# Performance work log

Hardware: AMD Instinct MI355X
Metric: run time of the kernel (lower is better)

The kernel has to match this reference:

```python
import jax, jax.numpy as jnp
import numpy as np

N = 100000   # nodes
E = 1600000  # edges (avg degree 16)
D = 128      # input feature dim
H = 128      # Config.hidden_dim
G = 64       # graphs in batch
OUT = 2      # output classes


def setup_inputs() -> dict:
    key = jax.random.key(0)
    ks = jax.random.split(key, 12)
    s = 0.05
    return {
        "x": jax.random.normal(ks[0], (N, D), dtype=jnp.float32),
        "edge_index": jax.random.randint(ks[1], (2, E), 0, N),
        "batch": jnp.sort(jax.random.randint(ks[2], (N,), 0, G)),
        "W1": jax.random.normal(ks[3], (H, D), dtype=jnp.float32) * s,
        "b1": jnp.zeros((H,), jnp.float32),
        "W2": jax.random.normal(ks[4], (H, H), dtype=jnp.float32) * s,
        "b2": jnp.zeros((H,), jnp.float32),
        "Wf1": jax.random.normal(ks[5], (H, H), dtype=jnp.float32) * s,
        "bf1": jnp.zeros((H,), jnp.float32),
        "Wf2": jax.random.normal(ks[6], (OUT, H), dtype=jnp.float32) * s,
        "bf2": jnp.zeros((OUT,), jnp.float32),
    }


def _gnn_layer(x, src, dst, W, b):
    # message(x_j) = Linear(x[src]); linear commutes with gather, so transform
    # node features once (N rows) instead of per-edge (E rows): same math.
    xw = x @ W.T + b                                   # [N, H]
    msg = xw[src]                                      # [E, H] gather
    summed = jax.ops.segment_sum(msg, dst, num_segments=N)            # [N, H]
    cnt = jax.ops.segment_sum(jnp.ones((src.shape[0],), x.dtype), dst,
                              num_segments=N)                          # [N]
    return summed / jnp.maximum(cnt, 1.0)[:, None]     # scatter-mean (0 for deg-0)


def reference(x, edge_index, batch, W1, b1, W2, b2, Wf1, bf1, Wf2, bf2):
    src, dst = edge_index[0], edge_index[1]
    h = jax.nn.relu(_gnn_layer(x, src, dst, W1, b1))
    h = jax.nn.relu(_gnn_layer(h, src, dst, W2, b2))
    g = jax.ops.segment_max(h, batch, num_segments=G)  # global_max_pool [G, H]
    z = jax.nn.relu(g @ Wf1.T + bf1)                   # fc (dropout = identity, eval)
    z = z @ Wf2.T + bf2                                # [G, OUT]
    return jax.nn.log_softmax(z, axis=1)
```

## Files before the change

kernel.cpp:

```cpp
#include <hip/hip_runtime.h>
#include <hip/hip_fp16.h>
#include <math.h>


#define SPLIT 16
#define BUCKET_SHIFT 8
#define BUCKET_SIZE 256
#define MAXBUCK 512
#define BIN_CHUNK 4096
#define CAP 4608
#define LSTR 136

typedef _Float16 half8 __attribute__((ext_vector_type(8)));
typedef _Float16 half4v __attribute__((ext_vector_type(4)));
typedef float floatx4 __attribute__((ext_vector_type(4)));
typedef float floatx2 __attribute__((ext_vector_type(2)));

__global__ void k_init(int* bcur, int* gstart, int* gend, int G, int nbuck) {
    int i = threadIdx.x;
    if (i < nbuck) bcur[i] = i * CAP;
    if (i < G) { gstart[i] = 0; gend[i] = 0; }
}

__global__ void k_bin(const int* __restrict__ src, const int* __restrict__ dst,
                      int* __restrict__ bcur, int* __restrict__ staging,
                      const int* __restrict__ batch, int* __restrict__ gstart,
                      int* __restrict__ gend, int E, int N, int nbuck) {
    __shared__ int lh[MAXBUCK];
    __shared__ int lbase[MAXBUCK];
    __shared__ int lc[MAXBUCK];
    int gid = blockIdx.x * blockDim.x + threadIdx.x;
    if (gid < N) {
        int b = batch[gid];
        if (gid == 0 || batch[gid - 1] != b) gstart[b] = gid;
        if (gid == N - 1 || batch[gid + 1] != b) gend[b] = gid + 1;
    }
    for (int i = threadIdx.x; i < nbuck; i += blockDim.x) { lh[i] = 0; lc[i] = 0; }
    __syncthreads();
    int base = blockIdx.x * BIN_CHUNK;
    int end = min(base + BIN_CHUNK, E);
    for (int e = base + threadIdx.x; e < end; e += blockDim.x)
        atomicAdd(&lh[dst[e] >> BUCKET_SHIFT], 1);
    __syncthreads();
    for (int i = threadIdx.x; i < nbuck; i += blockDim.x)
        if (lh[i]) lbase[i] = atomicAdd(&bcur[i], lh[i]);
    __syncthreads();
    for (int e = base + threadIdx.x; e < end; e += blockDim.x) {
        int d = dst[e];
        int b = d >> BUCKET_SHIFT;
        int pos = lbase[b] + atomicAdd(&lc[b], 1);
        if (pos < (b + 1) * CAP)
            staging[pos] = src[e] | ((d & (BUCKET_SIZE - 1)) << 24);
    }
}

__global__ __launch_bounds__(BUCKET_SIZE) void k_bcsr(
        const int* __restrict__ staging, const int* __restrict__ bcur,
        int* __restrict__ esrc, int* __restrict__ rowstart,
        int* __restrict__ deg, int N) {
    __shared__ int lh[BUCKET_SIZE];
    __shared__ int lrs[BUCKET_SIZE];
    __shared__ int lcur[BUCKET_SIZE];
    int b = blockIdx.x;
    int s = b * CAP;
    int e = min(bcur[b], s + CAP);
    int t = threadIdx.x;
    lh[t] = 0;
    __syncthreads();
    for (int i = s + t; i < e; i += BUCKET_SIZE)
        atomicAdd(&lh[((unsigned)staging[i]) >> 24], 1);
    __syncthreads();
    int v = lh[t];
    lrs[t] = v;
    __syncthreads();
    for (int off = 1; off < BUCKET_SIZE; off <<= 1) {
        int x = (t >= off) ? lrs[t - off] : 0;
        __syncthreads();
        lrs[t] += x;
        __syncthreads();
    }
    int excl = lrs[t] - v;
    int node = b * BUCKET_SIZE + t;
    if (node < N) { rowstart[node] = s + excl; deg[node] = v; }
    lcur[t] = excl;
    __syncthreads();
    for (int i = s + t; i < e; i += BUCKET_SIZE) {
        int p = staging[i];
        int local = ((unsigned)p) >> 24;
        int pos = atomicAdd(&lcur[local], 1);
        esrc[s + pos] = p & 0xFFFFFF;
    }
}

template <typename T>
__global__ __launch_bounds__(512) void k_gemm(const T* __restrict__ in,
                                              const float* __restrict__ W,
                                              const float* __restrict__ bias,
                                              unsigned char* __restrict__ out8,
                                              int N) {
    __shared__ _Float16 sX[128 * LSTR];
    __shared__ _Float16 sW[128 * LSTR];
    int t = threadIdx.x;
    int n0 = blockIdx.x * 128;

    #pragma unroll
    for (int it = 0; it < 8; ++it) {
        int lin = it * 512 + t;
        int r = lin >> 5;
        int c = (lin & 31) * 4;
        half4v xh;
        int n = n0 + r;
        if (n < N) {
            if constexpr (sizeof(T) == 4) {
                float4 xv = *(const float4*)((const float*)in + (size_t)n * 128 + c);
                xh = half4v{ (_Float16)xv.x, (_Float16)xv.y, (_Float16)xv.z, (_Float16)xv.w };
            } else {
                xh = *(const half4v*)((const _Float16*)in + (size_t)n * 128 + c);
            }
        } else {
            xh = half4v{ 0, 0, 0, 0 };
        }
        float4 wv = *(const float4*)(W + r * 128 + c);
        half4v wh = { (_Float16)wv.x, (_Float16)wv.y, (_Float16)wv.z, (_Float16)wv.w };
        *(half4v*)&sX[r * LSTR + c] = xh;
        *(half4v*)&sW[r * LSTR + c] = wh;
    }
    __syncthreads();

    int w = t >> 6;
    int lane = t & 63;
    int quad = lane >> 4;
    int lrow = lane & 15;

    floatx4 acc[8];
    #pragma unroll
    for (int i = 0; i < 8; ++i) acc[i] = {0.f, 0.f, 0.f, 0.f};

    int arow = (w * 16 + lrow) * LSTR + quad * 8;
    #pragma unroll
    for (int k0 = 0; k0 < 128; k0 += 32) {
        half8 a = *(const half8*)&sX[arow + k0];
        #pragma unroll
        for (int ht = 0; ht < 8; ++ht) {
            half8 b = *(const half8*)&sW[(ht * 16 + lrow) * LSTR + quad * 8 + k0];
            acc[ht] = __builtin_amdgcn_mfma_f32_16x16x32_f16(a, b, acc[ht], 0, 0, 0);
        }
    }

    #pragma unroll
    for (int ht = 0; ht < 8; ++ht) {
        int h = ht * 16 + lrow;
        float bv = bias[h];
        #pragma unroll
        for (int r = 0; r < 4; ++r) {
            int node = n0 + w * 16 + quad * 4 + r;
            if (node < N) {
                float v = acc[ht][r] + bv;
                int pk = __builtin_amdgcn_cvt_pk_fp8_f32(v, v, 0, false);
                out8[(size_t)node * 128 + h] = (unsigned char)(pk & 0xFF);
            }
        }
    }
}

__global__ __launch_bounds__(256) void k_agg(const unsigned char* __restrict__ in8,
                                             const int* __restrict__ esrc,
                                             const int* __restrict__ rowstart,
                                             const int* __restrict__ deg,
                                             _Float16* __restrict__ outh, int N) {
    int wv = __builtin_amdgcn_readfirstlane(threadIdx.x >> 6);
    int node = blockIdx.x * 4 + wv;
    if (node >= N) return;
    int lane = threadIdx.x & 63;
    int half = lane >> 5;
    unsigned voff = (lane & 31) * 4;
    int start = __builtin_amdgcn_readfirstlane(rowstart[node]);
    int d = __builtin_amdgcn_readfirstlane(deg[node]);

    floatx2 a0lo = {0.f, 0.f}, a0hi = {0.f, 0.f};
    floatx2 a1lo = {0.f, 0.f}, a1hi = {0.f, 0.f};
    int i = 0;
    for (; i + 4 <= d; i += 4) {
        int e0 = esrc[start + i];
        int e1 = esrc[start + i + 1];
        int e2 = esrc[start + i + 2];
        int e3 = esrc[start + i + 3];
        unsigned s01 = (unsigned)(half ? e1 : e0);
        unsigned s23 = (unsigned)(half ? e3 : e2);
        unsigned u0 = *(const unsigned*)(in8 + ((size_t)s01 << 7) + voff);
        unsigned u1 = *(const unsigned*)(in8 + ((size_t)s23 << 7) + voff);
        a0lo += __builtin_amdgcn_cvt_pk_f32_fp8(u0, false);
        a0hi += __builtin_amdgcn_cvt_pk_f32_fp8(u0, true);
        a1lo += __builtin_amdgcn_cvt_pk_f32_fp8(u1, false);
        a1hi += __builtin_amdgcn_cvt_pk_f32_fp8(u1, true);
    }
    for (; i + 2 <= d; i += 2) {
        int e0 = esrc[start + i];
        int e1 = esrc[start + i + 1];
        unsigned s01 = (unsigned)(half ? e1 : e0);
        unsigned u0 = *(const unsigned*)(in8 + ((size_t)s01 << 7) + voff);
        a0lo += __builtin_amdgcn_cvt_pk_f32_fp8(u0, false);
        a0hi += __builtin_amdgcn_cvt_pk_f32_fp8(u0, true);
    }
    if (i < d) {
        int e0 = esrc[start + i];
        unsigned u0 = *(const unsigned*)(in8 + ((size_t)e0 << 7) + voff);
        floatx2 lo = __builtin_amdgcn_cvt_pk_f32_fp8(u0, false);
        floatx2 hi = __builtin_amdgcn_cvt_pk_f32_fp8(u0, true);
        if (half == 0) { a0lo += lo; a0hi += hi; }
    }
    floatx2 slo = a0lo + a1lo;
    floatx2 shi = a0hi + a1hi;
    float c0 = slo.x + __shfl_down(slo.x, 32);
    float c1 = slo.y + __shfl_down(slo.y, 32);
    float c2 = shi.x + __shfl_down(shi.x, 32);
    float c3 = shi.y + __shfl_down(shi.y, 32);
    if (half == 0) {
        float dm = fmaxf((float)d, 1.0f);
        half4v r = { (_Float16)fmaxf(c0 / dm, 0.f),
                     (_Float16)fmaxf(c1 / dm, 0.f),
                     (_Float16)fmaxf(c2 / dm, 0.f),
                     (_Float16)fmaxf(c3 / dm, 0.f) };
        *(half4v*)(outh + (size_t)node * 128 + (lane & 31) * 4) = r;
    }
}

__global__ void k_pool1(const _Float16* __restrict__ h, const int* __restrict__ gstart,
                        const int* __restrict__ gend, float* __restrict__ pm, int G) {
    int g = blockIdx.x / SPLIT;
    int c = blockIdx.x % SPLIT;
    int t = threadIdx.x;
    int s = gstart[g], e = gend[g];
    int len = e - s;
    int chunk = (len + SPLIT - 1) / SPLIT;
    int lo = s + c * chunk;
    int hi = min(lo + chunk, e);
    float m = -INFINITY;
    for (int n = lo; n < hi; ++n)
        m = fmaxf(m, (float)h[(size_t)n * 128 + t]);
    pm[((size_t)g * SPLIT + c) * 128 + t] = m;
}

__global__ void k_fc(const float* __restrict__ pm,
                     const float* __restrict__ Wf1, const float* __restrict__ bf1,
                     const float* __restrict__ Wf2, const float* __restrict__ bf2,
                     float* __restrict__ out) {
    __shared__ float sg[128];
    __shared__ float sz[128];
    __shared__ float so[2];
    int g = blockIdx.x;
    int t = threadIdx.x;
    float m = -INFINITY;
    #pragma unroll
    for (int c = 0; c < SPLIT; ++c)
        m = fmaxf(m, pm[((size_t)g * SPLIT + c) * 128 + t]);
    sg[t] = m;
    __syncthreads();
    float z = bf1[t];
    #pragma unroll 4
    for (int d = 0; d < 128; ++d)
        z += sg[d] * Wf1[t * 128 + d];
    sz[t] = fmaxf(z, 0.f);
    __syncthreads();
    if (t < 2) {
        float o = bf2[t];
        for (int d = 0; d < 128; ++d)
            o += sz[d] * Wf2[t * 128 + d];
        so[t] = o;
    }
    __syncthreads();
    if (t == 0) {
        float a = so[0], b = so[1];
        float mx = fmaxf(a, b);
        float ls = mx + logf(expf(a - mx) + expf(b - mx));
        out[g * 2 + 0] = a - ls;
        out[g * 2 + 1] = b - ls;
    }
}

extern "C" void kernel_launch(void* const* d_in, const int* in_sizes, int n_in,
                              void* d_out, int out_size, void* d_ws, size_t ws_size,
                              hipStream_t stream) {
    const float* x   = (const float*)d_in[0];
    const int*   ei  = (const int*)d_in[1];
    const int* batch = (const int*)d_in[2];
    const float* W1  = (const float*)d_in[3];
    const float* b1  = (const float*)d_in[4];
    const float* W2  = (const float*)d_in[5];
    const float* b2  = (const float*)d_in[6];
    const float* Wf1 = (const float*)d_in[7];
    const float* bf1 = (const float*)d_in[8];
    const float* Wf2 = (const float*)d_in[9];
    const float* bf2 = (const float*)d_in[10];

    int N = in_sizes[2];
    int E = in_sizes[1] / 2;
    int G = out_size / 2;
    const int* src = ei;
    const int* dst = ei + E;
    int nbuck = (N + BUCKET_SIZE - 1) / BUCKET_SIZE;

    char* p = (char*)d_ws;
    auto alloc = [&](size_t bytes) -> char* {
        char* r = p;
        p += (bytes + 255) & ~(size_t)255;
        return r;
    };
    unsigned char* A = (unsigned char*)alloc((size_t)N * 128);
    _Float16* B    = (_Float16*)alloc((size_t)N * 128 * 2);
    int* deg       = (int*)alloc((size_t)N * 4);
    int* rowstart  = (int*)alloc((size_t)N * 4);
    int* esrc      = (int*)alloc((size_t)nbuck * CAP * 4);
    int* staging   = (int*)alloc((size_t)nbuck * CAP * 4);
    int* bcur      = (int*)alloc((MAXBUCK + 2) * 4);
    int* gstart    = (int*)alloc((size_t)G * 4);
    int* gend      = (int*)alloc((size_t)G * 4);
    float* pm      = (float*)alloc((size_t)G * SPLIT * 128 * 4);

    int nchunk = (E + BIN_CHUNK - 1) / BIN_CHUNK;

    k_init<<<1, MAXBUCK, 0, stream>>>(bcur, gstart, gend, G, nbuck);
    k_bin<<<nchunk, 256, 0, stream>>>(src, dst, bcur, staging, batch,
                                      gstart, gend, E, N, nbuck);
    k_bcsr<<<nbuck, BUCKET_SIZE, 0, stream>>>(staging, bcur, esrc, rowstart, deg, N);

    k_gemm<float><<<(N + 127) / 128, 512, 0, stream>>>(x, W1, b1, A, N);
    k_agg<<<(N + 3) / 4, 256, 0, stream>>>(A, esrc, rowstart, deg, B, N);
    k_gemm<_Float16><<<(N + 127) / 128, 512, 0, stream>>>(B, W2, b2, A, N);
    k_agg<<<(N + 3) / 4, 256, 0, stream>>>(A, esrc, rowstart, deg, B, N);
    k_pool1<<<G * SPLIT, 128, 0, stream>>>(B, gstart, gend, pm, G);
    k_fc<<<G, 128, 0, stream>>>(pm, Wf1, bf1, Wf2, bf2, (float*)d_out);
}
```

Baseline: 315.4 us.

## Fuse global max-pool into second aggregation via atomicMax and unroll gather

The second aggregation now pools directly into a per-graph buffer with integer atomicMax on float bits. Because all values are non-negative after ReLU and the buffer is zero-initialised, this ordering is valid. This removes the pool kernel, the fp16 write and re-read of the layer-2 output, and the graph boundary detection. The aggregation loop is also unrolled to 8 edges with four accumulator pairs, the tail is simplified, and blocks grow to 8 waves. The cost is atomic contention on the 64x128 pool buffer, since many nodes share the same graph.

```diff
diff --git a/kernel.cpp b/kernel.cpp
--- a/kernel.cpp
+++ b/kernel.cpp
@@ -3,7 +3,6 @@
 #include <math.h>
 
 
-#define SPLIT 16
 #define BUCKET_SHIFT 8
 #define BUCKET_SIZE 256
 #define MAXBUCK 512
@@ -16,25 +15,18 @@
 typedef float floatx4 __attribute__((ext_vector_type(4)));
 typedef float floatx2 __attribute__((ext_vector_type(2)));
 
-__global__ void k_init(int* bcur, int* gstart, int* gend, int G, int nbuck) {
-    int i = threadIdx.x;
+__global__ void k_init(int* bcur, float* pm, int nbuck, int pmn) {
+    int i = blockIdx.x * blockDim.x + threadIdx.x;
     if (i < nbuck) bcur[i] = i * CAP;
-    if (i < G) { gstart[i] = 0; gend[i] = 0; }
+    if (i < pmn) pm[i] = 0.f;
 }
 
 __global__ void k_bin(const int* __restrict__ src, const int* __restrict__ dst,
                       int* __restrict__ bcur, int* __restrict__ staging,
-                      const int* __restrict__ batch, int* __restrict__ gstart,
-                      int* __restrict__ gend, int E, int N, int nbuck) {
+                      int E, int nbuck) {
     __shared__ int lh[MAXBUCK];
     __shared__ int lbase[MAXBUCK];
     __shared__ int lc[MAXBUCK];
-    int gid = blockIdx.x * blockDim.x + threadIdx.x;
-    if (gid < N) {
-        int b = batch[gid];
-        if (gid == 0 || batch[gid - 1] != b) gstart[b] = gid;
-        if (gid == N - 1 || batch[gid + 1] != b) gend[b] = gid + 1;
-    }
     for (int i = threadIdx.x; i < nbuck; i += blockDim.x) { lh[i] = 0; lc[i] = 0; }
     __syncthreads();
     int base = blockIdx.x * BIN_CHUNK;
@@ -163,82 +155,83 @@
     }
 }
 
-__global__ __launch_bounds__(256) void k_agg(const unsigned char* __restrict__ in8,
+template <bool FUSE>
+__global__ __launch_bounds__(512) void k_agg(const unsigned char* __restrict__ in8,
                                              const int* __restrict__ esrc,
                                              const int* __restrict__ rowstart,
                                              const int* __restrict__ deg,
-                                             _Float16* __restrict__ outh, int N) {
+                                             _Float16* __restrict__ outh,
+                                             const int* __restrict__ batch,
+                                             float* __restrict__ pm, int N) {
     int wv = __builtin_amdgcn_readfirstlane(threadIdx.x >> 6);
-    int node = blockIdx.x * 4 + wv;
+    int node = blockIdx.x * 8 + wv;
     if (node >= N) return;
     int lane = threadIdx.x & 63;
-    int half = lane >> 5;
+    int hf = lane >> 5;
     unsigned voff = (lane & 31) * 4;
     int start = __builtin_amdgcn_readfirstlane(rowstart[node]);
     int d = __builtin_amdgcn_readfirstlane(deg[node]);
 
-    floatx2 a0lo = {0.f, 0.f}, a0hi = {0.f, 0.f};
-    floatx2 a1lo = {0.f, 0.f}, a1hi = {0.f, 0.f};
+    floatx2 a0lo = {0.f,0.f}, a0hi = {0.f,0.f};
+    floatx2 a1lo = {0.f,0.f}, a1hi = {0.f,0.f};
+    floatx2 a2lo = {0.f,0.f}, a2hi = {0.f,0.f};
+    floatx2 a3lo = {0.f,0.f}, a3hi = {0.f,0.f};
     int i = 0;
-    for (; i + 4 <= d; i += 4) {
+    for (; i + 8 <= d; i += 8) {
         int e0 = esrc[start + i];
         int e1 = esrc[start + i + 1];
         int e2 = esrc[start + i + 2];
         int e3 = esrc[start + i + 3];
-        unsigned s01 = (unsigned)(half ? e1 : e0);
-        unsigned s23 = (unsigned)(half ? e3 : e2);
-        unsigned u0 = *(const unsigned*)(in8 + ((size_t)s01 << 7) + voff);
-        unsigned u1 = *(const unsigned*)(in8 + ((size_t)s23 << 7) + voff);
+        int e4 = esrc[start + i + 4];
+        int e5 = esrc[start + i + 5];
+        int e6 = esrc[start + i + 6];
+        int e7 = esrc[start + i + 7];
+        unsigned u0 = *(const unsigned*)(in8 + ((size_t)(unsigned)(hf ? e1 : e0) << 7) + voff);
+        unsigned u1 = *(const unsigned*)(in8 + ((size_t)(unsigned)(hf ? e3 : e2) << 7) + voff);
+        unsigned u2 = *(const unsigned*)(in8 + ((size_t)(unsigned)(hf ? e5 : e4) << 7) + voff);
+        unsigned u3 = *(const unsigned*)(in8 + ((size_t)(unsigned)(hf ? e7 : e6) << 7) + voff);
         a0lo += __builtin_amdgcn_cvt_pk_f32_fp8(u0, false);
         a0hi += __builtin_amdgcn_cvt_pk_f32_fp8(u0, true);
         a1lo += __builtin_amdgcn_cvt_pk_f32_fp8(u1, false);
         a1hi += __builtin_amdgcn_cvt_pk_f32_fp8(u1, true);
-    }
-    for (; i + 2 <= d; i += 2) {
-        int e0 = esrc[start + i];
-        int e1 = esrc[start + i + 1];
-        unsigned s01 = (unsigned)(half ? e1 : e0);
-        unsigned u0 = *(const unsigned*)(in8 + ((size_t)s01 << 7) + voff);
-        a0lo += __builtin_amdgcn_cvt_pk_f32_fp8(u0, false);
-        a0hi += __builtin_amdgcn_cvt_pk_f32_fp8(u0, true);
-    }
-    if (i < d) {
-        int e0 = esrc[start + i];
-        unsigned u0 = *(const unsigned*)(in8 + ((size_t)e0 << 7) + voff);
-        floatx2 lo = __builtin_amdgcn_cvt_pk_f32_fp8(u0, false);
-        floatx2 hi = __builtin_amdgcn_cvt_pk_f32_fp8(u0, true);
-        if (half == 0) { a0lo += lo; a0hi += hi; }
-    }
-    floatx2 slo = a0lo + a1lo;
-    floatx2 shi = a0hi + a1hi;
+        a2lo += __builtin_amdgcn_cvt_pk_f32_fp8(u2, false);
+        a2hi += __builtin_amdgcn_cvt_pk_f32_fp8(u2, true);
+        a3lo += __builtin_amdgcn_cvt_pk_f32_fp8(u3, false);
+        a3hi += __builtin_amdgcn_cvt_pk_f32_fp8(u3, true);
+    }
+    for (; i < d; i += 2) {
+        int idxe = i + hf;
+        int cl = min(idxe, d - 1);
+        int e = esrc[start + cl];
+        unsigned u = *(const unsigned*)(in8 + ((size_t)(unsigned)e << 7) + voff);
+        if (idxe >= d) u = 0u;
+        a0lo += __builtin_amdgcn_cvt_pk_f32_fp8(u, false);
+        a0hi += __builtin_amdgcn_cvt_pk_f32_fp8(u, true);
+    }
+    floatx2 slo = (a0lo + a1lo) + (a2lo + a3lo);
+    floatx2 shi = (a0hi + a1hi) + (a2hi + a3hi);
     float c0 = slo.x + __shfl_down(slo.x, 32);
     float c1 = slo.y + __shfl_down(slo.y, 32);
     float c2 = shi.x + __shfl_down(shi.x, 32);
     float c3 = shi.y + __shfl_down(shi.y, 32);
-    if (half == 0) {
+    if (hf == 0) {
         float dm = fmaxf((float)d, 1.0f);
-        half4v r = { (_Float16)fmaxf(c0 / dm, 0.f),
-                     (_Float16)fmaxf(c1 / dm, 0.f),
-                     (_Float16)fmaxf(c2 / dm, 0.f),
-                     (_Float16)fmaxf(c3 / dm, 0.f) };
-        *(half4v*)(outh + (size_t)node * 128 + (lane & 31) * 4) = r;
-    }
-}
-
-__global__ void k_pool1(const _Float16* __restrict__ h, const int* __restrict__ gstart,
-                        const int* __restrict__ gend, float* __restrict__ pm, int G) {
-    int g = blockIdx.x / SPLIT;
-    int c = blockIdx.x % SPLIT;
-    int t = threadIdx.x;
-    int s = gstart[g], e = gend[g];
-    int len = e - s;
-    int chunk = (len + SPLIT - 1) / SPLIT;
-    int lo = s + c * chunk;
-    int hi = min(lo + chunk, e);
-    float m = -INFINITY;
-    for (int n = lo; n < hi; ++n)
-        m = fmaxf(m, (float)h[(size_t)n * 128 + t]);
-    pm[((size_t)g * SPLIT + c) * 128 + t] = m;
+        float r0 = fmaxf(c0 / dm, 0.f);
+        float r1 = fmaxf(c1 / dm, 0.f);
+        float r2 = fmaxf(c2 / dm, 0.f);
+        float r3 = fmaxf(c3 / dm, 0.f);
+        if constexpr (FUSE) {
+            int g = __builtin_amdgcn_readfirstlane(batch[node]);
+            unsigned* pmrow = (unsigned*)(pm + (size_t)g * 128) + (lane & 31) * 4;
+            atomicMax(pmrow + 0, __float_as_uint(r0));
+            atomicMax(pmrow + 1, __float_as_uint(r1));
+            atomicMax(pmrow + 2, __float_as_uint(r2));
+            atomicMax(pmrow + 3, __float_as_uint(r3));
+        } else {
+            half4v r = { (_Float16)r0, (_Float16)r1, (_Float16)r2, (_Float16)r3 };
+            *(half4v*)(outh + (size_t)node * 128 + (lane & 31) * 4) = r;
+        }
+    }
 }
 
 __global__ void k_fc(const float* __restrict__ pm,
@@ -250,11 +243,7 @@
     __shared__ float so[2];
     int g = blockIdx.x;
     int t = threadIdx.x;
-    float m = -INFINITY;
-    #pragma unroll
-    for (int c = 0; c < SPLIT; ++c)
-        m = fmaxf(m, pm[((size_t)g * SPLIT + c) * 128 + t]);
-    sg[t] = m;
+    sg[t] = pm[(size_t)g * 128 + t];
     __syncthreads();
     float z = bf1[t];
     #pragma unroll 4
@@ -313,21 +302,19 @@
     int* esrc      = (int*)alloc((size_t)nbuck * CAP * 4);
     int* staging   = (int*)alloc((size_t)nbuck * CAP * 4);
     int* bcur      = (int*)alloc((MAXBUCK + 2) * 4);
-    int* gstart    = (int*)alloc((size_t)G * 4);
-    int* gend      = (int*)alloc((size_t)G * 4);
-    float* pm      = (float*)alloc((size_t)G * SPLIT * 128 * 4);
+    float* pm      = (float*)alloc((size_t)G * 128 * 4);
 
     int nchunk = (E + BIN_CHUNK - 1) / BIN_CHUNK;
 
-    k_init<<<1, MAXBUCK, 0, stream>>>(bcur, gstart, gend, G, nbuck);
-    k_bin<<<nchunk, 256, 0, stream>>>(src, dst, bcur, staging, batch,
-                                      gstart, gend, E, N, nbuck);
+    k_init<<<16, 512, 0, stream>>>(bcur, pm, nbuck, G * 128);
+    k_bin<<<nchunk, 256, 0, stream>>>(src, dst, bcur, staging, E, nbuck);
     k_bcsr<<<nbuck, BUCKET_SIZE, 0, stream>>>(staging, bcur, esrc, rowstart, deg, N);
 
     k_gemm<float><<<(N + 127) / 128, 512, 0, stream>>>(x, W1, b1, A, N);
-    k_agg<<<(N + 3) / 4, 256, 0, stream>>>(A, esrc, rowstart, deg, B, N);
+    k_agg<false><<<(N + 7) / 8, 512, 0, stream>>>(A, esrc, rowstart, deg, B,
+                                                  batch, pm, N);
     k_gemm<_Float16><<<(N + 127) / 128, 512, 0, stream>>>(B, W2, b2, A, N);
-    k_agg<<<(N + 3) / 4, 256, 0, stream>>>(A, esrc, rowstart, deg, B, N);
-    k_pool1<<<G * SPLIT, 128, 0, stream>>>(B, gstart, gend, pm, G);
+    k_agg<true><<<(N + 7) / 8, 512, 0, stream>>>(A, esrc, rowstart, deg, B,
+                                                 batch, pm, N);
     k_fc<<<G, 128, 0, stream>>>(pm, Wf1, bf1, Wf2, bf2, (float*)d_out);
 }
```

After: 747.3 us. 137% more time.
